# Optimization experiments

Hardware: AMD Instinct MI355X
Metric: run time of the kernel (lower is better)

The kernel has to match this reference:

```python
import jax, jax.numpy as jnp
import numpy as np

B, N, C = 8, 1024, 640   # frames, tokens per frame (32x32), channels
H, D = 8, 80             # heads, dim per head; inner = H*D = 640
R = 3                    # adaptive context_range (uniform, odd)
SCALE = D ** -0.5


def _window_indices(batch_size, context_range):
    """Replicates the per-sample index construction in RefAttention.forward.
    First half of the batch attends within [0, B//2-1], second within [B//2, B-1]."""
    half = batch_size // 2
    hr = (context_range - 1) // 2
    rows = []
    for i in range(batch_size):
        lo_b, hi_b = (0, half - 1) if i < half else (half, batch_size - 1)
        ci = list(range(max(lo_b, i - hr), min(hi_b, i + hr + 1)))  # arange(a, min(hi_b, i+hr+1))
        while len(ci) < context_range:
            if ci[0] > lo_b:
                ci = [ci[0] - 1] + ci
            if len(ci) < context_range and ci[-1] < hi_b:
                ci = ci + [ci[-1] + 1]
        rows.append(ci)
    return np.asarray(rows, dtype=np.int32)  # [B, R]


def setup_inputs() -> dict:
    key = jax.random.key(0)
    ks = jax.random.split(key, 6)
    inner = H * D
    x = jax.random.normal(ks[0], (B, N, C), dtype=jnp.float32)
    s = 1.0 / np.sqrt(C)
    Wq = jax.random.normal(ks[1], (inner, C), dtype=jnp.float32) * s
    Wk = jax.random.normal(ks[2], (inner, C), dtype=jnp.float32) * s
    Wv = jax.random.normal(ks[3], (inner, C), dtype=jnp.float32) * s
    Wo = jax.random.normal(ks[4], (C, inner), dtype=jnp.float32) * (1.0 / np.sqrt(inner))
    bo = jnp.zeros((C,), dtype=jnp.float32)
    ctx_idx = jnp.asarray(_window_indices(B, R))  # [B, R] int32, static window gather indices
    return {"x": x, "Wq": Wq, "Wk": Wk, "Wv": Wv, "Wo": Wo, "bo": bo, "ctx_idx": ctx_idx}


def reference(x, Wq, Wk, Wv, Wo, bo, ctx_idx):
    # projections (nn.Linear, no bias): y = x @ W^T
    q = jnp.einsum('bnc,ic->bni', x, Wq)                      # [B, N, inner]
    k = jnp.einsum('bnc,ic->bni', x, Wk)                      # context defaults to x
    v = jnp.einsum('bnc,ic->bni', x, Wv)
    # original uses k.data / v.data (detached); forward value is identical
    qh = q.reshape(B, N, H, D)
    # gather per-frame K/V windows: [B, R, N, inner] -> [B, R*N, H, D]
    kw = k[ctx_idx].reshape(B, R * N, H, D)
    vw = v[ctx_idx].reshape(B, R * N, H, D)
    sim = jnp.einsum('bnhd,bmhd->bhnm', qh, kw) * SCALE       # [B, H, N, R*N]
    attn = jax.nn.softmax(sim, axis=-1)
    out = jnp.einsum('bhnm,bmhd->bnhd', attn, vw).reshape(B, N, H * D)
    return jnp.einsum('bni,ci->bnc', out, Wo) + bo            # to_out (dropout p=0)
```

## Files before the change

### kernel.cpp

```cpp
#include <hip/hip_runtime.h>
#include <hip/hip_bf16.h>

#define BB    8
#define NNTOK 1024
#define CCH   640
#define HH    8
#define DHD   80
#define RRW   3
#define MM    (BB * NNTOK)
#define INNER 640
#define SCALE 0.111803398874989484820458954f
#define QSCALE (SCALE * 1.44269504088896340736f)

#define KSTR 88
#define VSTR 72
#define ESTR 136

typedef __bf16 bf16x8 __attribute__((ext_vector_type(8)));
typedef float  f32x4  __attribute__((ext_vector_type(4)));

__device__ __forceinline__ unsigned short f2b(float f) {
    union { float f; unsigned int u; } v; v.f = f;
    unsigned int r = v.u + 0x7fffu + ((v.u >> 16) & 1u);
    return (unsigned short)(r >> 16);
}
__device__ __forceinline__ bf16x8 zero8() {
    bf16x8 z;
#pragma unroll
    for (int i = 0; i < 8; i++) z[i] = (__bf16)0.0f;
    return z;
}
__device__ __forceinline__ f32x4 zero4() {
    f32x4 z;
#pragma unroll
    for (int i = 0; i < 4; i++) z[i] = 0.0f;
    return z;
}
__device__ __forceinline__ float fexp2(float x) {
#if __has_builtin(__builtin_amdgcn_exp2f)
    return __builtin_amdgcn_exp2f(x);
#else
    return __expf(x * 0.69314718055994530942f);
#endif
}

__global__ __launch_bounds__(256) void castk(const float* __restrict__ s,
                                             unsigned short* __restrict__ d, int n) {
    int i = (blockIdx.x * 256 + threadIdx.x) * 4;
    if (i < n) {
        float4 f = *(const float4*)(s + i);
        ushort4 o;
        o.x = f2b(f.x); o.y = f2b(f.y); o.z = f2b(f.z); o.w = f2b(f.w);
        *(ushort4*)(d + i) = o;
    }
}

__global__ __launch_bounds__(256) void castw4(
    const float* __restrict__ w0, const float* __restrict__ w1,
    const float* __restrict__ w2, const float* __restrict__ w3,
    unsigned short* __restrict__ d0, unsigned short* __restrict__ d1,
    unsigned short* __restrict__ d2, unsigned short* __restrict__ d3, int n)
{
    const float* s; unsigned short* d;
    switch (blockIdx.y) {
        case 0: s = w0; d = d0; break;
        case 1: s = w1; d = d1; break;
        case 2: s = w2; d = d2; break;
        default: s = w3; d = d3; break;
    }
    int i = (blockIdx.x * 256 + threadIdx.x) * 4;
    if (i < n) {
        float4 f = *(const float4*)(s + i);
        ushort4 o;
        o.x = f2b(f.x); o.y = f2b(f.y); o.z = f2b(f.z); o.w = f2b(f.w);
        *(ushort4*)(d + i) = o;
    }
}

__global__ __launch_bounds__(512, 4) void proj_qkv_mfma(
    const unsigned short* __restrict__ xb,
    const unsigned short* __restrict__ wqb,
    const unsigned short* __restrict__ wkb,
    const unsigned short* __restrict__ wvb,
    unsigned short* __restrict__ q16, unsigned short* __restrict__ k16,
    unsigned short* __restrict__ vto)
{
    __shared__ __align__(16) unsigned short Sh[2 * 128 * 72];
    unsigned short* Xs  = Sh;
    unsigned short* Wsh = Sh + 128 * 72;
    const int t = threadIdx.x;
    const int wvid = t >> 6, lane = t & 63, col = lane & 15, quad = lane >> 4;
    const int wrow = wvid & 3, wcol = wvid >> 2;
    const int m0 = blockIdx.x * 128, i0 = blockIdx.y * 128, z = blockIdx.z;
    const unsigned short* W = (z == 0) ? wqb : (z == 1) ? wkb : wvb;
    const int srow = t >> 3, sseg = t & 7;

    f32x4 accA[4], accB[4];
#pragma unroll
    for (int nt = 0; nt < 4; nt++) { accA[nt] = zero4(); accB[nt] = zero4(); }

    for (int kt = 0; kt < INNER; kt += 64) {
        uint4 x0 = *(const uint4*)(xb + (size_t)(m0 + srow) * INNER + kt + sseg * 8);
        uint4 x1 = *(const uint4*)(xb + (size_t)(m0 + 64 + srow) * INNER + kt + sseg * 8);
        uint4 w0 = *(const uint4*)(W  + (size_t)(i0 + srow) * INNER + kt + sseg * 8);
        uint4 w1 = *(const uint4*)(W  + (size_t)(i0 + 64 + srow) * INNER + kt + sseg * 8);
        __syncthreads();
        *(uint4*)&Xs[srow * 72 + sseg * 8]        = x0;
        *(uint4*)&Xs[(64 + srow) * 72 + sseg * 8] = x1;
        *(uint4*)&Wsh[srow * 72 + sseg * 8]        = w0;
        *(uint4*)&Wsh[(64 + srow) * 72 + sseg * 8] = w1;
        __syncthreads();
#pragma unroll
        for (int kbk = 0; kbk < 2; kbk++) {
            bf16x8 afA = *(const bf16x8*)&Xs[(wrow * 32 + col) * 72 + kbk * 32 + quad * 8];
            bf16x8 afB = *(const bf16x8*)&Xs[(wrow * 32 + 16 + col) * 72 + kbk * 32 + quad * 8];
#pragma unroll
            for (int nt = 0; nt < 4; nt++) {
                bf16x8 bfr = *(const bf16x8*)&Wsh[(wcol * 64 + nt * 16 + col) * 72 + kbk * 32 + quad * 8];
                accA[nt] = __builtin_amdgcn_mfma_f32_16x16x32_bf16(afA, bfr, accA[nt], 0, 0, 0);
                accB[nt] = __builtin_amdgcn_mfma_f32_16x16x32_bf16(afB, bfr, accB[nt], 0, 0, 0);
            }
        }
    }
    __syncthreads();
    unsigned short* Ts = Sh;
    const int rA = wrow * 32 + quad * 4;
    if (z != 2) {
        const float sc = (z == 0) ? QSCALE : 1.0f;
#pragma unroll
        for (int nt = 0; nt < 4; nt++) {
            const int ci = wcol * 64 + nt * 16 + col;
#pragma unroll
            for (int r = 0; r < 4; r++) {
                Ts[(rA + r) * ESTR + ci]      = f2b(accA[nt][r] * sc);
                Ts[(rA + 16 + r) * ESTR + ci] = f2b(accB[nt][r] * sc);
            }
        }
        __syncthreads();
        unsigned short* dst = (z == 0) ? q16 : k16;
#pragma unroll
        for (int j = 0; j < 4; j++) {
            const int idx = t + 512 * j, row = idx >> 4, seg = idx & 15;
            uint4 v = *(const uint4*)&Ts[row * ESTR + seg * 8];
            *(uint4*)(dst + (size_t)(m0 + row) * INNER + i0 + seg * 8) = v;
        }
    } else {
#pragma unroll
        for (int nt = 0; nt < 4; nt++) {
            const int ci = wcol * 64 + nt * 16 + col;
#pragma unroll
            for (int r = 0; r < 4; r++) {
                Ts[ci * ESTR + rA + r]      = f2b(accA[nt][r]);
                Ts[ci * ESTR + rA + 16 + r] = f2b(accB[nt][r]);
            }
        }
        __syncthreads();
        const int bfm = m0 >> 10, n0 = m0 & (NNTOK - 1);
#pragma unroll
        for (int j = 0; j < 4; j++) {
            const int idx = t + 512 * j, li = idx >> 4, seg = idx & 15;
            const int i = i0 + li;
            const int h = i / DHD, dd = i % DHD;
            uint4 v = *(const uint4*)&Ts[li * ESTR + seg * 8];
            *(uint4*)(vto + ((size_t)(bfm * HH + h) * DHD + dd) * NNTOK + n0 + seg * 8) = v;
        }
    }
}

__device__ __forceinline__ int ksrow(int tau) {
    return (((tau >> 5) * 2 + ((tau >> 2) & 1)) << 4) + (((tau >> 3) & 3) << 2) + (tau & 3);
}

__global__ __launch_bounds__(256, 2) void attn_mfma10(
    const unsigned short* __restrict__ qb, const unsigned short* __restrict__ kb,
    const unsigned short* __restrict__ vt, const int* __restrict__ ctx,
    unsigned short* __restrict__ ao)
{
    __shared__ __align__(16) unsigned short Ks[2][64 * KSTR];
    __shared__ __align__(16) unsigned short Vt[2][DHD * VSTR];
    const int t = threadIdx.x;
    const int wvid = t >> 6, lane = t & 63, col = lane & 15, quad = lane >> 4;
    const int qt = blockIdx.x, h = blockIdx.y, b = blockIdx.z;

    bf16x8 qfA0, qfA1, qfA2, qfB0, qfB1, qfB2;
    {
        const unsigned short* qpA = qb + (size_t)(b * NNTOK + qt * 128 + wvid * 32 + col) * INNER + h * DHD;
        const unsigned short* qpB = qpA + (size_t)16 * INNER;
        qfA0 = *(const bf16x8*)(qpA + quad * 8);
        qfA1 = *(const bf16x8*)(qpA + 32 + quad * 8);
        qfB0 = *(const bf16x8*)(qpB + quad * 8);
        qfB1 = *(const bf16x8*)(qpB + 32 + quad * 8);
        qfA2 = zero8(); qfB2 = zero8();
        if (quad < 2) {
            qfA2 = *(const bf16x8*)(qpA + 64 + quad * 8);
            qfB2 = *(const bf16x8*)(qpB + 64 + quad * 8);
        }
    }
    f32x4 oA[5], oB[5];
#pragma unroll
    for (int dt = 0; dt < 5; dt++) { oA[dt] = zero4(); oB[dt] = zero4(); }
    float lpA = 0.0f, lpB = 0.0f;

    const int i0 = t, i1 = t + 256, i2 = t + 512;
    const int ktok0 = i0 / 10, kseg0 = i0 % 10, ksr0 = ksrow(ktok0);
    const int ktok1 = i1 / 10, kseg1 = i1 % 10, ksr1 = ksrow(ktok1);
    const int ktok2 = i2 / 10, kseg2 = i2 % 10, ksr2 = ksrow(ktok2);
    const int vd0 = i0 >> 3, vs0 = i0 & 7;
    const int vd1 = i1 >> 3, vs1 = i1 & 7;
    const int vd2 = i2 >> 3, vs2 = i2 & 7;

    {
        const int fr = ctx[b * RRW];
        const unsigned short* kbase = kb + (size_t)(fr * NNTOK) * INNER + h * DHD;
        const unsigned short* vbase = vt + ((size_t)(fr * HH + h) * DHD) * NNTOK;
        uint4 ka0 = *(const uint4*)(kbase + (size_t)ktok0 * INNER + kseg0 * 8);
        uint4 ka1 = *(const uint4*)(kbase + (size_t)ktok1 * INNER + kseg1 * 8);
        uint4 va0 = *(const uint4*)(vbase + (size_t)vd0 * NNTOK + vs0 * 8);
        uint4 va1 = *(const uint4*)(vbase + (size_t)vd1 * NNTOK + vs1 * 8);
        *(uint4*)&Ks[0][ksr0 * KSTR + kseg0 * 8] = ka0;
        *(uint4*)&Ks[0][ksr1 * KSTR + kseg1 * 8] = ka1;
        *(uint4*)&Vt[0][vd0 * VSTR + vs0 * 8] = va0;
        *(uint4*)&Vt[0][vd1 * VSTR + vs1 * 8] = va1;
        if (t < 128) {
            uint4 ka2 = *(const uint4*)(kbase + (size_t)ktok2 * INNER + kseg2 * 8);
            uint4 va2 = *(const uint4*)(vbase + (size_t)vd2 * NNTOK + vs2 * 8);
            *(uint4*)&Ks[0][ksr2 * KSTR + kseg2 * 8] = ka2;
            *(uint4*)&Vt[0][vd2 * VSTR + vs2 * 8] = va2;
        }
    }

    for (int kc = 0; kc < (RRW * NNTOK) / 64; kc++) {
        __syncthreads();

        const int kcn = (kc + 1 < 48) ? kc + 1 : 47;
        const int frn = ctx[b * RRW + (kcn >> 4)];
        const int tokn = (kcn & 15) * 64;
        const unsigned short* kbase = kb + (size_t)(frn * NNTOK + tokn) * INNER + h * DHD;
        const unsigned short* vbase = vt + ((size_t)(frn * HH + h) * DHD) * NNTOK + tokn;
        uint4 ka0 = *(const uint4*)(kbase + (size_t)ktok0 * INNER + kseg0 * 8);
        uint4 ka1 = *(const uint4*)(kbase + (size_t)ktok1 * INNER + kseg1 * 8);
        uint4 va0 = *(const uint4*)(vbase + (size_t)vd0 * NNTOK + vs0 * 8);
        uint4 va1 = *(const uint4*)(vbase + (size_t)vd1 * NNTOK + vs1 * 8);
        uint4 ka2, va2;
        if (t < 128) {
            ka2 = *(const uint4*)(kbase + (size_t)ktok2 * INNER + kseg2 * 8);
            va2 = *(const uint4*)(vbase + (size_t)vd2 * NNTOK + vs2 * 8);
        }

        const unsigned short* ksr = &Ks[kc & 1][0];
        const unsigned short* vtr = &Vt[kc & 1][0];

        f32x4 sA[4], sB[4];
        __builtin_amdgcn_s_setprio(1);
#pragma unroll
        for (int n0 = 0; n0 < 4; n0++) {
            const unsigned short* kp = ksr + (n0 * 16 + col) * KSTR;
            bf16x8 k0 = *(const bf16x8*)(kp + quad * 8);
            bf16x8 k1 = *(const bf16x8*)(kp + 32 + quad * 8);
            bf16x8 k2 = zero8();
            if (quad < 2) k2 = *(const bf16x8*)(kp + 64 + quad * 8);
            f32x4 svA = zero4(), svB = zero4();
            svA = __builtin_amdgcn_mfma_f32_16x16x32_bf16(k0, qfA0, svA, 0, 0, 0);
            svB = __builtin_amdgcn_mfma_f32_16x16x32_bf16(k0, qfB0, svB, 0, 0, 0);
            svA = __builtin_amdgcn_mfma_f32_16x16x32_bf16(k1, qfA1, svA, 0, 0, 0);
            svB = __builtin_amdgcn_mfma_f32_16x16x32_bf16(k1, qfB1, svB, 0, 0, 0);
            svA = __builtin_amdgcn_mfma_f32_16x16x32_bf16(k2, qfA2, svA, 0, 0, 0);
            svB = __builtin_amdgcn_mfma_f32_16x16x32_bf16(k2, qfB2, svB, 0, 0, 0);
            sA[n0] = svA; sB[n0] = svB;
        }
        __builtin_amdgcn_s_setprio(0);
        bf16x8 paA0, paA1, paB0, paB1;
#pragma unroll
        for (int n0 = 0; n0 < 4; n0++) {
            const int j0 = (n0 & 1) * 4;
            float a0 = fexp2(sA[n0][0]), a1 = fexp2(sA[n0][1]);
            float a2 = fexp2(sA[n0][2]), a3 = fexp2(sA[n0][3]);
            lpA += (a0 + a1) + (a2 + a3);
            float b0 = fexp2(sB[n0][0]), b1 = fexp2(sB[n0][1]);
            float b2 = fexp2(sB[n0][2]), b3 = fexp2(sB[n0][3]);
            lpB += (b0 + b1) + (b2 + b3);
            if (n0 < 2) {
                paA0[j0] = (__bf16)a0; paA0[j0+1] = (__bf16)a1; paA0[j0+2] = (__bf16)a2; paA0[j0+3] = (__bf16)a3;
                paB0[j0] = (__bf16)b0; paB0[j0+1] = (__bf16)b1; paB0[j0+2] = (__bf16)b2; paB0[j0+3] = (__bf16)b3;
            } else {
                paA1[j0] = (__bf16)a0; paA1[j0+1] = (__bf16)a1; paA1[j0+2] = (__bf16)a2; paA1[j0+3] = (__bf16)a3;
                paB1[j0] = (__bf16)b0; paB1[j0+1] = (__bf16)b1; paB1[j0+2] = (__bf16)b2; paB1[j0+3] = (__bf16)b3;
            }
        }
        __builtin_amdgcn_s_setprio(1);
#pragma unroll
        for (int dt = 0; dt < 5; dt++) {
            const unsigned short* vp = vtr + (dt * 16 + col) * VSTR;
            bf16x8 v0 = *(const bf16x8*)(vp + quad * 8);
            bf16x8 v1 = *(const bf16x8*)(vp + 32 + quad * 8);
            oA[dt] = __builtin_amdgcn_mfma_f32_16x16x32_bf16(paA0, v0, oA[dt], 0, 0, 0);
            oB[dt] = __builtin_amdgcn_mfma_f32_16x16x32_bf16(paB0, v0, oB[dt], 0, 0, 0);
            oA[dt] = __builtin_amdgcn_mfma_f32_16x16x32_bf16(paA1, v1, oA[dt], 0, 0, 0);
            oB[dt] = __builtin_amdgcn_mfma_f32_16x16x32_bf16(paB1, v1, oB[dt], 0, 0, 0);
        }
        __builtin_amdgcn_s_setprio(0);
        {
            unsigned short* ksb = &Ks[(kc + 1) & 1][0];
            unsigned short* vtb = &Vt[(kc + 1) & 1][0];
            *(uint4*)&ksb[ksr0 * KSTR + kseg0 * 8] = ka0;
            *(uint4*)&ksb[ksr1 * KSTR + kseg1 * 8] = ka1;
            *(uint4*)&vtb[vd0 * VSTR + vs0 * 8] = va0;
            *(uint4*)&vtb[vd1 * VSTR + vs1 * 8] = va1;
            if (t < 128) {
                *(uint4*)&ksb[ksr2 * KSTR + kseg2 * 8] = ka2;
                *(uint4*)&vtb[vd2 * VSTR + vs2 * 8] = va2;
            }
        }
    }
    float lsA = lpA, lsB = lpB;
    lsA += __shfl_xor(lsA, 16); lsA += __shfl_xor(lsA, 32);
    lsB += __shfl_xor(lsB, 16); lsB += __shfl_xor(lsB, 32);
    float invA[4], invB[4];
#pragma unroll
    for (int r = 0; r < 4; r++) {
        invA[r] = 1.0f / __shfl(lsA, quad * 4 + r);
        invB[r] = 1.0f / __shfl(lsB, quad * 4 + r);
    }
#pragma unroll
    for (int r = 0; r < 4; r++) {
        unsigned short* opA = ao + (size_t)(b * NNTOK + qt * 128 + wvid * 32 + quad * 4 + r) * INNER + h * DHD;
        unsigned short* opB = opA + (size_t)16 * INNER;
#pragma unroll
        for (int dt = 0; dt < 5; dt++) {
            opA[dt * 16 + col] = f2b(oA[dt][r] * invA[r]);
            opB[dt * 16 + col] = f2b(oB[dt][r] * invB[r]);
        }
    }
}

__global__ __launch_bounds__(256) void proj_out_mfma(
    const unsigned short* __restrict__ ab, const unsigned short* __restrict__ wob,
    const float* __restrict__ bo, float* __restrict__ out)
{
    __shared__ __align__(16) unsigned short Xs[64 * 72];
    __shared__ __align__(16) unsigned short Wsh[64 * 72];
    const int t = threadIdx.x;
    const int wvid = t >> 6, lane = t & 63, col = lane & 15, quad = lane >> 4;
    const int m0 = blockIdx.x * 64, i0 = blockIdx.y * 64;
    const int row = t >> 2, seg = t & 3;

    float bias[4];
#pragma unroll
    for (int nt = 0; nt < 4; nt++) bias[nt] = bo[i0 + nt * 16 + col];

    f32x4 acc[4];
#pragma unroll
    for (int nt = 0; nt < 4; nt++) acc[nt] = zero4();

    for (int kt = 0; kt < INNER; kt += 64) {
        uint4 x0 = *(const uint4*)(ab  + (size_t)(m0 + row) * INNER + kt + seg * 16);
        uint4 x1 = *(const uint4*)(ab  + (size_t)(m0 + row) * INNER + kt + seg * 16 + 8);
        uint4 w0 = *(const uint4*)(wob + (size_t)(i0 + row) * INNER + kt + seg * 16);
        uint4 w1 = *(const uint4*)(wob + (size_t)(i0 + row) * INNER + kt + seg * 16 + 8);
        __syncthreads();
        *(uint4*)&Xs[row * 72 + seg * 16]      = x0;
        *(uint4*)&Xs[row * 72 + seg * 16 + 8]  = x1;
        *(uint4*)&Wsh[row * 72 + seg * 16]     = w0;
        *(uint4*)&Wsh[row * 72 + seg * 16 + 8] = w1;
        __syncthreads();
#pragma unroll
        for (int kbk = 0; kbk < 2; kbk++) {
            bf16x8 af = *(const bf16x8*)&Xs[(wvid * 16 + col) * 72 + kbk * 32 + quad * 8];
#pragma unroll
            for (int nt = 0; nt < 4; nt++) {
                bf16x8 bfr = *(const bf16x8*)&Wsh[(nt * 16 + col) * 72 + kbk * 32 + quad * 8];
                acc[nt] = __builtin_amdgcn_mfma_f32_16x16x32_bf16(af, bfr, acc[nt], 0, 0, 0);
            }
        }
    }
#pragma unroll
    for (int nt = 0; nt < 4; nt++)
#pragma unroll
        for (int r = 0; r < 4; r++)
            out[(size_t)(m0 + wvid * 16 + quad * 4 + r) * CCH + i0 + nt * 16 + col] = acc[nt][r] + bias[nt];
}

extern "C" void kernel_launch(void* const* d_in, const int* in_sizes, int n_in,
                              void* d_out, int out_size, void* d_ws, size_t ws_size,
                              hipStream_t stream) {
    const float* x  = (const float*)d_in[0];
    const float* wq = (const float*)d_in[1];
    const float* wk = (const float*)d_in[2];
    const float* wv = (const float*)d_in[3];
    const float* wo = (const float*)d_in[4];
    const float* bo = (const float*)d_in[5];
    const int* ctx  = (const int*)d_in[6];
    float* out = (float*)d_out;

    const size_t XN = (size_t)MM * INNER;
    const size_t WN = (size_t)INNER * CCH;
    unsigned short* q16 = (unsigned short*)d_ws;
    unsigned short* k16 = q16 + XN;
    unsigned short* vto = k16 + XN;
    unsigned short* xb  = vto + XN;
    unsigned short* aob = xb;
    unsigned short* wqb = xb + XN;
    unsigned short* wkb = wqb + WN;
    unsigned short* wvb = wkb + WN;
    unsigned short* wob = wvb + WN;

    castk<<<dim3((XN / 4 + 255) / 256), 256, 0, stream>>>(x, xb, (int)XN);
    castw4<<<dim3((WN / 4 + 255) / 256, 4), 256, 0, stream>>>(wq, wk, wv, wo, wqb, wkb, wvb, wob, (int)WN);

    proj_qkv_mfma<<<dim3(MM / 128, INNER / 128, 3), 512, 0, stream>>>(xb, wqb, wkb, wvb, q16, k16, vto);
    attn_mfma10<<<dim3(NNTOK / 128, HH, BB), 256, 0, stream>>>(q16, k16, vto, ctx, aob);
    proj_out_mfma<<<dim3(MM / 64, CCH / 64), 256, 0, stream>>>(aob, wob, bo, out);
}
```

Before: 207.5 us.

## Process four query subtiles per wave to raise K/V reuse in attention

The attention kernel now gives each wave 64 query rows (four 16-row subtiles) instead of 32, so each block covers 256 queries and the grid is halved. Each K/V tile loaded into shared memory is reused by twice as many queries, which halves K/V global traffic and LDS staging per query. The exp and P packing are also fused into the QK loop per subtile. The cost is roughly double the accumulator and Q-fragment registers, with launch bounds dropped to one block per SM, and only 256 blocks in the grid, which reduces occupancy and latency hiding.

```diff
diff --git a/kernel.cpp b/kernel.cpp
--- a/kernel.cpp
+++ b/kernel.cpp
@@ -171,7 +171,7 @@
     return (((tau >> 5) * 2 + ((tau >> 2) & 1)) << 4) + (((tau >> 3) & 3) << 2) + (tau & 3);
 }
 
-__global__ __launch_bounds__(256, 2) void attn_mfma10(
+__global__ __launch_bounds__(256, 1) void attn_mfma11(
     const unsigned short* __restrict__ qb, const unsigned short* __restrict__ kb,
     const unsigned short* __restrict__ vt, const int* __restrict__ ctx,
     unsigned short* __restrict__ ao)
@@ -182,24 +182,24 @@
     const int wvid = t >> 6, lane = t & 63, col = lane & 15, quad = lane >> 4;
     const int qt = blockIdx.x, h = blockIdx.y, b = blockIdx.z;
 
-    bf16x8 qfA0, qfA1, qfA2, qfB0, qfB1, qfB2;
+    bf16x8 qf0[4], qf1[4], qf2[4];
     {
-        const unsigned short* qpA = qb + (size_t)(b * NNTOK + qt * 128 + wvid * 32 + col) * INNER + h * DHD;
-        const unsigned short* qpB = qpA + (size_t)16 * INNER;
-        qfA0 = *(const bf16x8*)(qpA + quad * 8);
-        qfA1 = *(const bf16x8*)(qpA + 32 + quad * 8);
-        qfB0 = *(const bf16x8*)(qpB + quad * 8);
-        qfB1 = *(const bf16x8*)(qpB + 32 + quad * 8);
-        qfA2 = zero8(); qfB2 = zero8();
-        if (quad < 2) {
-            qfA2 = *(const bf16x8*)(qpA + 64 + quad * 8);
-            qfB2 = *(const bf16x8*)(qpB + 64 + quad * 8);
-        }
-    }
-    f32x4 oA[5], oB[5];
-#pragma unroll
-    for (int dt = 0; dt < 5; dt++) { oA[dt] = zero4(); oB[dt] = zero4(); }
-    float lpA = 0.0f, lpB = 0.0f;
+        const unsigned short* qp0 = qb + (size_t)(b * NNTOK + qt * 256 + wvid * 64 + col) * INNER + h * DHD;
+#pragma unroll
+        for (int s = 0; s < 4; s++) {
+            const unsigned short* qp = qp0 + (size_t)(s * 16) * INNER;
+            qf0[s] = *(const bf16x8*)(qp + quad * 8);
+            qf1[s] = *(const bf16x8*)(qp + 32 + quad * 8);
+            qf2[s] = zero8();
+            if (quad < 2) qf2[s] = *(const bf16x8*)(qp + 64 + quad * 8);
+        }
+    }
+    f32x4 o[4][5];
+#pragma unroll
+    for (int s = 0; s < 4; s++)
+#pragma unroll
+        for (int dt = 0; dt < 5; dt++) o[s][dt] = zero4();
+    float lp[4] = {0.0f, 0.0f, 0.0f, 0.0f};
 
     const int i0 = t, i1 = t + 256, i2 = t + 512;
     const int ktok0 = i0 / 10, kseg0 = i0 % 10, ksr0 = ksrow(ktok0);
@@ -250,7 +250,7 @@
         const unsigned short* ksr = &Ks[kc & 1][0];
         const unsigned short* vtr = &Vt[kc & 1][0];
 
-        f32x4 sA[4], sB[4];
+        bf16x8 pa0[4], pa1[4];
         __builtin_amdgcn_s_setprio(1);
 #pragma unroll
         for (int n0 = 0; n0 < 4; n0++) {
@@ -259,44 +259,37 @@
             bf16x8 k1 = *(const bf16x8*)(kp + 32 + quad * 8);
             bf16x8 k2 = zero8();
             if (quad < 2) k2 = *(const bf16x8*)(kp + 64 + quad * 8);
-            f32x4 svA = zero4(), svB = zero4();
-            svA = __builtin_amdgcn_mfma_f32_16x16x32_bf16(k0, qfA0, svA, 0, 0, 0);
-            svB = __builtin_amdgcn_mfma_f32_16x16x32_bf16(k0, qfB0, svB, 0, 0, 0);
-            svA = __builtin_amdgcn_mfma_f32_16x16x32_bf16(k1, qfA1, svA, 0, 0, 0);
-            svB = __builtin_amdgcn_mfma_f32_16x16x32_bf16(k1, qfB1, svB, 0, 0, 0);
-            svA = __builtin_amdgcn_mfma_f32_16x16x32_bf16(k2, qfA2, svA, 0, 0, 0);
-            svB = __builtin_amdgcn_mfma_f32_16x16x32_bf16(k2, qfB2, svB, 0, 0, 0);
-            sA[n0] = svA; sB[n0] = svB;
+            const int j0 = (n0 & 1) * 4;
+#pragma unroll
+            for (int s = 0; s < 4; s++) {
+                f32x4 sv = zero4();
+                sv = __builtin_amdgcn_mfma_f32_16x16x32_bf16(k0, qf0[s], sv, 0, 0, 0);
+                sv = __builtin_amdgcn_mfma_f32_16x16x32_bf16(k1, qf1[s], sv, 0, 0, 0);
+                sv = __builtin_amdgcn_mfma_f32_16x16x32_bf16(k2, qf2[s], sv, 0, 0, 0);
+                float p0 = fexp2(sv[0]), p1 = fexp2(sv[1]);
+                float p2 = fexp2(sv[2]), p3 = fexp2(sv[3]);
+                lp[s] += (p0 + p1) + (p2 + p3);
+                if (n0 < 2) {
+                    pa0[s][j0]   = (__bf16)p0; pa0[s][j0+1] = (__bf16)p1;
+                    pa0[s][j0+2] = (__bf16)p2; pa0[s][j0+3] = (__bf16)p3;
+                } else {
+                    pa1[s][j0]   = (__bf16)p0; pa1[s][j0+1] = (__bf16)p1;
+                    pa1[s][j0+2] = (__bf16)p2; pa1[s][j0+3] = (__bf16)p3;
+                }
+            }
         }
         __builtin_amdgcn_s_setprio(0);
-        bf16x8 paA0, paA1, paB0, paB1;
-#pragma unroll
-        for (int n0 = 0; n0 < 4; n0++) {
-            const int j0 = (n0 & 1) * 4;
-            float a0 = fexp2(sA[n0][0]), a1 = fexp2(sA[n0][1]);
-            float a2 = fexp2(sA[n0][2]), a3 = fexp2(sA[n0][3]);
-            lpA += (a0 + a1) + (a2 + a3);
-            float b0 = fexp2(sB[n0][0]), b1 = fexp2(sB[n0][1]);
-            float b2 = fexp2(sB[n0][2]), b3 = fexp2(sB[n0][3]);
-            lpB += (b0 + b1) + (b2 + b3);
-            if (n0 < 2) {
-                paA0[j0] = (__bf16)a0; paA0[j0+1] = (__bf16)a1; paA0[j0+2] = (__bf16)a2; paA0[j0+3] = (__bf16)a3;
-                paB0[j0] = (__bf16)b0; paB0[j0+1] = (__bf16)b1; paB0[j0+2] = (__bf16)b2; paB0[j0+3] = (__bf16)b3;
-            } else {
-                paA1[j0] = (__bf16)a0; paA1[j0+1] = (__bf16)a1; paA1[j0+2] = (__bf16)a2; paA1[j0+3] = (__bf16)a3;
-                paB1[j0] = (__bf16)b0; paB1[j0+1] = (__bf16)b1; paB1[j0+2] = (__bf16)b2; paB1[j0+3] = (__bf16)b3;
-            }
-        }
         __builtin_amdgcn_s_setprio(1);
 #pragma unroll
         for (int dt = 0; dt < 5; dt++) {
             const unsigned short* vp = vtr + (dt * 16 + col) * VSTR;
             bf16x8 v0 = *(const bf16x8*)(vp + quad * 8);
             bf16x8 v1 = *(const bf16x8*)(vp + 32 + quad * 8);
-            oA[dt] = __builtin_amdgcn_mfma_f32_16x16x32_bf16(paA0, v0, oA[dt], 0, 0, 0);
-            oB[dt] = __builtin_amdgcn_mfma_f32_16x16x32_bf16(paB0, v0, oB[dt], 0, 0, 0);
-            oA[dt] = __builtin_amdgcn_mfma_f32_16x16x32_bf16(paA1, v1, oA[dt], 0, 0, 0);
-            oB[dt] = __builtin_amdgcn_mfma_f32_16x16x32_bf16(paB1, v1, oB[dt], 0, 0, 0);
+#pragma unroll
+            for (int s = 0; s < 4; s++) {
+                o[s][dt] = __builtin_amdgcn_mfma_f32_16x16x32_bf16(pa0[s], v0, o[s][dt], 0, 0, 0);
+                o[s][dt] = __builtin_amdgcn_mfma_f32_16x16x32_bf16(pa1[s], v1, o[s][dt], 0, 0, 0);
+            }
         }
         __builtin_amdgcn_s_setprio(0);
         {
@@ -312,23 +305,25 @@
             }
         }
     }
-    float lsA = lpA, lsB = lpB;
-    lsA += __shfl_xor(lsA, 16); lsA += __shfl_xor(lsA, 32);
-    lsB += __shfl_xor(lsB, 16); lsB += __shfl_xor(lsB, 32);
-    float invA[4], invB[4];
-#pragma unroll
-    for (int r = 0; r < 4; r++) {
-        invA[r] = 1.0f / __shfl(lsA, quad * 4 + r);
-        invB[r] = 1.0f / __shfl(lsB, quad * 4 + r);
-    }
-#pragma unroll
-    for (int r = 0; r < 4; r++) {
-        unsigned short* opA = ao + (size_t)(b * NNTOK + qt * 128 + wvid * 32 + quad * 4 + r) * INNER + h * DHD;
-        unsigned short* opB = opA + (size_t)16 * INNER;
-#pragma unroll
-        for (int dt = 0; dt < 5; dt++) {
-            opA[dt * 16 + col] = f2b(oA[dt][r] * invA[r]);
-            opB[dt * 16 + col] = f2b(oB[dt][r] * invB[r]);
+#pragma unroll
+    for (int s = 0; s < 4; s++) {
+        float ls = lp[s];
+        ls += __shfl_xor(ls, 16);
+        ls += __shfl_xor(ls, 32);
+        lp[s] = ls;
+    }
+#pragma unroll
+    for (int s = 0; s < 4; s++) {
+        float inv[4];
+#pragma unroll
+        for (int r = 0; r < 4; r++)
+            inv[r] = 1.0f / __shfl(lp[s], quad * 4 + r);
+#pragma unroll
+        for (int r = 0; r < 4; r++) {
+            unsigned short* op = ao + (size_t)(b * NNTOK + qt * 256 + wvid * 64 + s * 16 + quad * 4 + r) * INNER + h * DHD;
+#pragma unroll
+            for (int dt = 0; dt < 5; dt++)
+                op[dt * 16 + col] = f2b(o[s][dt][r] * inv[r]);
         }
     }
 }
@@ -408,6 +403,6 @@
     castw4<<<dim3((WN / 4 + 255) / 256, 4), 256, 0, stream>>>(wq, wk, wv, wo, wqb, wkb, wvb, wob, (int)WN);
 
     proj_qkv_mfma<<<dim3(MM / 128, INNER / 128, 3), 512, 0, stream>>>(xb, wqb, wkb, wvb, q16, k16, vto);
-    attn_mfma10<<<dim3(NNTOK / 128, HH, BB), 256, 0, stream>>>(q16, k16, vto, ctx, aob);
+    attn_mfma11<<<dim3(NNTOK / 256, HH, BB), 256, 0, stream>>>(q16, k16, vto, ctx, aob);
     proj_out_mfma<<<dim3(MM / 64, CCH / 64), 256, 0, stream>>>(aob, wob, bo, out);
 }
```

New measurement: 224.6 us. 8.3% more time.
